# Kernel optimization log

Measured on AMD Instinct MI355X. Metric: run time of the kernel, lower is better.

Reference implementation:

```python
import jax, jax.numpy as jnp
import numpy as np

N = 50000
E = 800000
D_IN, D_HID, D_OUT = 128, 128, 64


def setup_inputs() -> dict:
    key = jax.random.key(0)
    ks = jax.random.split(key, 8)
    x = jax.random.normal(ks[0], (N, D_IN), dtype=jnp.float32)
    edge_index = jax.random.randint(ks[1], (2, E), 0, N, dtype=jnp.int64)
    # Glorot-ish init for GCNConv linear weights + zero bias (PyG default bias=True)
    def lin(k, din, dout):
        s = 1.0 / np.sqrt(din)
        return jax.random.uniform(k, (din, dout), jnp.float32, -s, s)
    return {
        "x": x,
        "edge_index": edge_index,
        "W1": lin(ks[2], D_IN, D_HID), "b1": jnp.zeros((D_HID,), jnp.float32),
        "W2": lin(ks[3], D_HID, D_HID), "b2": jnp.zeros((D_HID,), jnp.float32),
        "W3": lin(ks[4], D_HID, D_OUT), "b3": jnp.zeros((D_OUT,), jnp.float32),
    }


def _prep_edges(edge_index, n):
    # add self loops (PyG GCNConv default add_self_loops=True)
    loop = jnp.arange(n, dtype=edge_index.dtype)
    src = jnp.concatenate([edge_index[0], loop])
    dst = jnp.concatenate([edge_index[1], loop])
    deg = jax.ops.segment_sum(jnp.ones_like(dst, dtype=jnp.float32), dst, num_segments=n)
    dinv = jnp.where(deg > 0, jax.lax.rsqrt(deg), 0.0)
    norm = dinv[src] * dinv[dst]  # symmetric normalization per edge
    return src, dst, norm


def _gcn_conv(h, W, b, src, dst, norm, n):
    h = h @ W                                   # [N, dout]
    msg = h[src] * norm[:, None]                # [E+N, dout] gather
    out = jax.ops.segment_sum(msg, dst, num_segments=n)  # scatter-add
    return out + b


def reference(x, edge_index, W1, b1, W2, b2, W3, b3):
    src, dst, norm = _prep_edges(edge_index, N)
    h = jax.nn.relu(_gcn_conv(x, W1, b1, src, dst, norm, N))
    h = jax.nn.relu(_gcn_conv(h, W2, b2, src, dst, norm, N))
    return _gcn_conv(h, W3, b3, src, dst, norm, N)  # eval mode: dropout is identity
```

## Files before the change

### kernel.cpp

```cpp
#include <hip/hip_runtime.h>
#include <hip/hip_fp16.h>
#include <math.h>

#define NN 50000
#define NE 800000
#define RAWSTRIDE 96
#define NBUCK 196
#define NBBIN 196
#define BCAP 4608
#define ACH 4096
#define G1B 782

using bf8v = __attribute__((ext_vector_type(8))) short;
using f4v  = __attribute__((ext_vector_type(4))) float;
using u32x4 = __attribute__((ext_vector_type(4))) unsigned int;
using u32x2 = __attribute__((ext_vector_type(2))) unsigned int;

__device__ inline unsigned short f2bf(float f) {
    unsigned int u = __float_as_uint(f);
    u += 0x7FFFu + ((u >> 16) & 1u);
    return (unsigned short)(u >> 16);
}
__device__ inline float bflo(unsigned int d) { return __uint_as_float(d << 16); }
__device__ inline float bfhi(unsigned int d) { return __uint_as_float(d & 0xFFFF0000u); }

__device__ inline uint4 ntload4(const void* p) {
    u32x4 v = __builtin_nontemporal_load((const u32x4*)p);
    return make_uint4(v[0], v[1], v[2], v[3]);
}
__device__ inline void ntstore4(void* p, uint4 v) {
    u32x4 x; x[0] = v.x; x[1] = v.y; x[2] = v.z; x[3] = v.w;
    __builtin_nontemporal_store(x, (u32x4*)p);
}
__device__ inline void ntstore2(void* p, uint2 v) {
    u32x2 x; x[0] = v.x; x[1] = v.y;
    __builtin_nontemporal_store(x, (u32x2*)p);
}


__device__ __forceinline__ void bin_body(const int* __restrict__ src,
                                         const int* __restrict__ dst,
                                         int* __restrict__ gcursor,
                                         unsigned int* __restrict__ bst,
                                         int bx, char* shc) {
    unsigned int* items = (unsigned int*)shc;
    int* cnt    = (int*)(shc + 16384);
    int* pref   = (int*)(shc + 17408);
    int* gstart = (int*)(shc + 18436);
    const int t = threadIdx.x;
    cnt[t] = 0;
    __syncthreads();
    const int base = bx * ACH;

    unsigned int my[16]; int myb[16], myr[16];
    #pragma unroll
    for (int i = 0; i < 16; ++i) {
        int e = base + i * 256 + t;
        my[i] = 0; myb[i] = -1; myr[i] = 0;
        if (e < NE) {
            int d = __builtin_nontemporal_load(dst + e);
            int s = __builtin_nontemporal_load(src + e);
            my[i] = (unsigned int)s | ((unsigned int)d << 16);
            int b = d >> 8;
            myb[i] = b;
            myr[i] = atomicAdd(&cnt[b], 1);
        }
    }
    __syncthreads();
    {
        int* scanb = (int*)items;
        scanb[t] = cnt[t];
        __syncthreads();
        #pragma unroll
        for (int off = 1; off < 256; off <<= 1) {
            int v = (t >= off) ? scanb[t - off] : 0;
            __syncthreads();
            scanb[t] += v;
            __syncthreads();
        }
        if (t == 0) pref[0] = 0;
        pref[t + 1] = scanb[t];
    }
    __syncthreads();
    if (cnt[t] > 0) gstart[t] = atomicAdd(&gcursor[t], cnt[t]);
    __syncthreads();
    #pragma unroll
    for (int i = 0; i < 16; ++i)
        if (myb[i] >= 0) items[pref[myb[i]] + myr[i]] = my[i];
    __syncthreads();
    const int total = pref[256];
    for (int i = t; i < total; i += 256) {
        int lo = 0, hi = 255;
        while (lo < hi) { int mid = (lo + hi + 1) >> 1; if (pref[mid] <= i) lo = mid; else hi = mid - 1; }
        int idx = gstart[lo] + (i - pref[lo]);
        if (idx < BCAP) __builtin_nontemporal_store(items[i], &bst[(size_t)lo * BCAP + idx]);
    }
}


__global__ __launch_bounds__(512) void sortb_kernel(const int* __restrict__ gcursor,
                                                    const unsigned int* __restrict__ bst,
                                                    int* __restrict__ cnt_g,
                                                    float* __restrict__ dinv,
                                                    unsigned short* __restrict__ raw) {
    __shared__ unsigned int items[BCAP];
    __shared__ int cnt[256], pref[257], cur[256], scanb[256];
    __shared__ unsigned short outl[BCAP];
    const int b = blockIdx.x;
    const int t = threadIdx.x;
    int n = gcursor[b];
    if (n > BCAP) n = BCAP;
    if (t < 256) { cnt[t] = 0; cur[t] = 0; }
    __syncthreads();
    for (int i = t; i < n; i += 512) {
        unsigned int u = __builtin_nontemporal_load(&bst[(size_t)b * BCAP + i]);
        items[i] = u;
        atomicAdd(&cnt[(u >> 16) & 255], 1);
    }
    __syncthreads();
    if (t < 256) scanb[t] = cnt[t];
    __syncthreads();
    #pragma unroll
    for (int off = 1; off < 256; off <<= 1) {
        int v = 0;
        if (t < 256 && t >= off) v = scanb[t - off];
        __syncthreads();
        if (t < 256) scanb[t] += v;
        __syncthreads();
    }
    if (t == 0) pref[0] = 0;
    if (t < 256) pref[t + 1] = scanb[t];
    __syncthreads();
    for (int i = t; i < n; i += 512) {
        unsigned int u = items[i];
        int ln = (u >> 16) & 255;
        int r = atomicAdd(&cur[ln], 1);
        outl[pref[ln] + r] = (unsigned short)(u & 0xFFFFu);
    }
    __syncthreads();
    for (int i = t; i < n; i += 512) {
        int lo = 0, hi = 255;
        while (lo < hi) { int mid = (lo + hi + 1) >> 1; if (pref[mid] <= i) lo = mid; else hi = mid - 1; }
        int r = i - pref[lo];
        if (r < RAWSTRIDE)
            __builtin_nontemporal_store(outl[i], &raw[(size_t)(b * 256 + lo) * RAWSTRIDE + r]);
    }
    if (t < 256) {
        int node = b * 256 + t;
        if (node < NN) {
            int c = cnt[t];
            cnt_g[node] = c;
            dinv[node] = rsqrtf((float)(1 + c));
        }
    }
}


__device__ __forceinline__ void gemm128_body_f32(const float* __restrict__ A,
                                                 const float* __restrict__ W,
                                                 unsigned short* __restrict__ out,
                                                 int bx, char* shc) {
    unsigned short* Wt = (unsigned short*)shc;
    unsigned short* Dt = (unsigned short*)(shc + 128 * 136 * 2);
    const int t = threadIdx.x;
    const int row0 = bx * 64;

    {
        int n = t & 127;
        int kbase = (t >> 7) * 4;
        for (int kk = kbase; kk < 128; kk += 8) {
            float w0 = W[(kk + 0) * 128 + n];
            float w1 = W[(kk + 1) * 128 + n];
            float w2 = W[(kk + 2) * 128 + n];
            float w3 = W[(kk + 3) * 128 + n];
            unsigned int p0 = (unsigned int)f2bf(w0) | ((unsigned int)f2bf(w1) << 16);
            unsigned int p1 = (unsigned int)f2bf(w2) | ((unsigned int)f2bf(w3) << 16);
            *(unsigned int*)&Wt[n * 136 + kk]     = p0;
            *(unsigned int*)&Wt[n * 136 + kk + 2] = p1;
        }
    }
    __syncthreads();

    const int wave = t >> 6;
    const int lane = t & 63;
    const int m16  = lane & 15;
    const int quad = lane >> 4;
    const int arow = row0 + wave * 16 + m16;
    const int arowc = (arow < NN) ? arow : 0;

    f4v acc[8];
    #pragma unroll
    for (int i = 0; i < 8; ++i) acc[i] = (f4v)(0.0f);

    #pragma unroll
    for (int k0 = 0; k0 < 128; k0 += 32) {
        bf8v afrag;
        const float4* ap = (const float4*)(A + (size_t)arowc * 128 + k0 + quad * 8);
        float4 a0 = ap[0], a1 = ap[1];
        afrag[0] = (short)f2bf(a0.x); afrag[1] = (short)f2bf(a0.y);
        afrag[2] = (short)f2bf(a0.z); afrag[3] = (short)f2bf(a0.w);
        afrag[4] = (short)f2bf(a1.x); afrag[5] = (short)f2bf(a1.y);
        afrag[6] = (short)f2bf(a1.z); afrag[7] = (short)f2bf(a1.w);
        #pragma unroll
        for (int nt = 0; nt < 8; ++nt) {
            bf8v bfrag = *(const bf8v*)&Wt[(nt * 16 + m16) * 136 + k0 + quad * 8];
            acc[nt] = __builtin_amdgcn_mfma_f32_16x16x32_bf16(afrag, bfrag, acc[nt], 0, 0, 0);
        }
    }

    #pragma unroll
    for (int nt = 0; nt < 8; ++nt) {
        #pragma unroll
        for (int r = 0; r < 4; ++r) {
            Dt[(wave * 16 + quad * 4 + r) * 136 + nt * 16 + m16] = f2bf(acc[nt][r]);
        }
    }
    __syncthreads();

    {
        int r = t >> 2;
        int c = t & 3;
        int gr = row0 + r;
        if (gr < NN) {
            const uint4* s = (const uint4*)&Dt[r * 136] + c * 4;
            uint4* d = (uint4*)(out + (size_t)gr * 128) + c * 4;
            ntstore4(d + 0, s[0]); ntstore4(d + 1, s[1]);
            ntstore4(d + 2, s[2]); ntstore4(d + 3, s[3]);
        }
    }
}

__global__ __launch_bounds__(256) void bin_g1_kernel(const int* __restrict__ src,
                                                     const int* __restrict__ dst,
                                                     int* __restrict__ gcursor,
                                                     unsigned int* __restrict__ bst,
                                                     const float* __restrict__ x,
                                                     const float* __restrict__ W1,
                                                     unsigned short* __restrict__ hb) {
    __shared__ __align__(16) char sh[52224];
    if (blockIdx.x < NBBIN) {
        bin_body(src, dst, gcursor, bst, blockIdx.x, sh);
    } else {
        gemm128_body_f32(x, W1, hb, blockIdx.x - NBBIN, sh);
    }
}


#define ACC8(G, W_) \
    acc[0] += W_ * bflo(G.x); acc[1] += W_ * bfhi(G.x); \
    acc[2] += W_ * bflo(G.y); acc[3] += W_ * bfhi(G.y); \
    acc[4] += W_ * bflo(G.z); acc[5] += W_ * bfhi(G.z); \
    acc[6] += W_ * bflo(G.w); acc[7] += W_ * bfhi(G.w);

#define AGG128_BODY(HV, RROW, C, DIW, LANE)                                         \
    {                                                                               \
        uint4 g = HV[(size_t)wid * 16 + (LANE)];                                    \
        float ws = (DIW) * (DIW);                                                   \
        acc[0] = ws * bflo(g.x); acc[1] = ws * bfhi(g.x);                           \
        acc[2] = ws * bflo(g.y); acc[3] = ws * bfhi(g.y);                           \
        acc[4] = ws * bflo(g.z); acc[5] = ws * bfhi(g.z);                           \
        acc[6] = ws * bflo(g.w); acc[7] = ws * bfhi(g.w);                           \
    }                                                                               \
    const int cfull = (C) & ~7;                                                     \
    uint4 q;                                                                        \
    if (cfull > 0) q = ntload4(RROW);                                               \
    for (int e = 0; e < cfull; e += 8) {                                            \
        uint4 qc = q;                                                               \
        if (e + 8 < cfull) q = ntload4((RROW) + e + 8);                             \
        int c0 = qc.x & 0xFFFFu, c1 = qc.x >> 16;                                   \
        int c2 = qc.y & 0xFFFFu, c3 = qc.y >> 16;                                   \
        int c4 = qc.z & 0xFFFFu, c5 = qc.z >> 16;                                   \
        int c6 = qc.w & 0xFFFFu, c7 = qc.w >> 16;                                   \
        uint4 g0 = HV[(size_t)c0 * 16 + (LANE)];                                    \
        uint4 g1 = HV[(size_t)c1 * 16 + (LANE)];                                    \
        uint4 g2 = HV[(size_t)c2 * 16 + (LANE)];                                    \
        uint4 g3 = HV[(size_t)c3 * 16 + (LANE)];                                    \
        uint4 g4 = HV[(size_t)c4 * 16 + (LANE)];                                    \
        uint4 g5 = HV[(size_t)c5 * 16 + (LANE)];                                    \
        uint4 g6 = HV[(size_t)c6 * 16 + (LANE)];                                    \
        uint4 g7 = HV[(size_t)c7 * 16 + (LANE)];                                    \
        float w0 = (DIW) * dinv[c0], w1 = (DIW) * dinv[c1];                         \
        float w2 = (DIW) * dinv[c2], w3 = (DIW) * dinv[c3];                         \
        float w4 = (DIW) * dinv[c4], w5 = (DIW) * dinv[c5];                         \
        float w6 = (DIW) * dinv[c6], w7 = (DIW) * dinv[c7];                         \
        ACC8(g0, w0) ACC8(g1, w1) ACC8(g2, w2) ACC8(g3, w3)                         \
        ACC8(g4, w4) ACC8(g5, w5) ACC8(g6, w6) ACC8(g7, w7)                         \
    }                                                                               \
    if ((C) & 7) {                                                                  \
        int e = cfull, rem = (C) - e;                                               \
        uint4 qc = ntload4((RROW) + e);                                             \
        int c0 = qc.x & 0xFFFFu, c1 = qc.x >> 16;                                   \
        int c2 = qc.y & 0xFFFFu, c3 = qc.y >> 16;                                   \
        int c4 = qc.z & 0xFFFFu, c5 = qc.z >> 16;                                   \
        int c6 = qc.w & 0xFFFFu, c7 = qc.w >> 16;                                   \
        if (rem <= 1) c1 = 0; if (rem <= 2) c2 = 0; if (rem <= 3) c3 = 0;           \
        if (rem <= 4) c4 = 0; if (rem <= 5) c5 = 0; if (rem <= 6) c6 = 0;           \
        c7 = 0;                                                                     \
        float w0 = (DIW) * dinv[c0];                                                \
        float w1 = (rem > 1) ? (DIW) * dinv[c1] : 0.f;                              \
        float w2 = (rem > 2) ? (DIW) * dinv[c2] : 0.f;                              \
        float w3 = (rem > 3) ? (DIW) * dinv[c3] : 0.f;                              \
        float w4 = (rem > 4) ? (DIW) * dinv[c4] : 0.f;                              \
        float w5 = (rem > 5) ? (DIW) * dinv[c5] : 0.f;                              \
        float w6 = (rem > 6) ? (DIW) * dinv[c6] : 0.f;                              \
        float w7 = 0.f;                                                             \
        uint4 g0 = HV[(size_t)c0 * 16 + (LANE)];                                    \
        uint4 g1 = HV[(size_t)c1 * 16 + (LANE)];                                    \
        uint4 g2 = HV[(size_t)c2 * 16 + (LANE)];                                    \
        uint4 g3 = HV[(size_t)c3 * 16 + (LANE)];                                    \
        uint4 g4 = HV[(size_t)c4 * 16 + (LANE)];                                    \
        uint4 g5 = HV[(size_t)c5 * 16 + (LANE)];                                    \
        uint4 g6 = HV[(size_t)c6 * 16 + (LANE)];                                    \
        uint4 g7 = HV[(size_t)c7 * 16 + (LANE)];                                    \
        ACC8(g0, w0) ACC8(g1, w1) ACC8(g2, w2) ACC8(g3, w3)                         \
        ACC8(g4, w4) ACC8(g5, w5) ACC8(g6, w6) ACC8(g7, w7)                         \
    }


__global__ __launch_bounds__(256) void aggW2_kernel(const unsigned short* __restrict__ hin,
                                                    const unsigned short* __restrict__ raw,
                                                    const int* __restrict__ cnt_g,
                                                    const float* __restrict__ dinv,
                                                    const float* __restrict__ bias,
                                                    const float* __restrict__ W,
                                                    unsigned short* __restrict__ out) {
    __shared__ unsigned short Wt[128 * 136];
    __shared__ unsigned short Zt[64 * 136];
    const int t = threadIdx.x;
    const int row0 = blockIdx.x * 64;

    {
        int n = t & 127;
        int kbase = (t >> 7) * 4;
        for (int kk = kbase; kk < 128; kk += 8) {
            float w0 = W[(kk + 0) * 128 + n];
            float w1 = W[(kk + 1) * 128 + n];
            float w2 = W[(kk + 2) * 128 + n];
            float w3 = W[(kk + 3) * 128 + n];
            unsigned int p0 = (unsigned int)f2bf(w0) | ((unsigned int)f2bf(w1) << 16);
            unsigned int p1 = (unsigned int)f2bf(w2) | ((unsigned int)f2bf(w3) << 16);
            *(unsigned int*)&Wt[n * 136 + kk]     = p0;
            *(unsigned int*)&Wt[n * 136 + kk + 2] = p1;
        }
    }

    const int group = t >> 4;
    const int lane  = t & 15;
    const uint4* hv = (const uint4*)hin;
    const float4* bp = (const float4*)bias;
    float4 b0 = bp[lane * 2], b1 = bp[lane * 2 + 1];

    for (int r = 0; r < 4; ++r) {
        const int wid = row0 + r * 16 + group;
        uint4 o = make_uint4(0u, 0u, 0u, 0u);
        if (wid < NN) {
            int c = cnt_g[wid];
            if (c > RAWSTRIDE) c = RAWSTRIDE;
            const float diw = dinv[wid];
            const unsigned short* rrow = raw + (size_t)wid * RAWSTRIDE;
            float acc[8];
            AGG128_BODY(hv, rrow, c, diw, lane)
            acc[0] += b0.x; acc[1] += b0.y; acc[2] += b0.z; acc[3] += b0.w;
            acc[4] += b1.x; acc[5] += b1.y; acc[6] += b1.z; acc[7] += b1.w;
            #pragma unroll
            for (int j = 0; j < 8; ++j) acc[j] = fmaxf(acc[j], 0.f);
            o.x = (unsigned int)f2bf(acc[0]) | ((unsigned int)f2bf(acc[1]) << 16);
            o.y = (unsigned int)f2bf(acc[2]) | ((unsigned int)f2bf(acc[3]) << 16);
            o.z = (unsigned int)f2bf(acc[4]) | ((unsigned int)f2bf(acc[5]) << 16);
            o.w = (unsigned int)f2bf(acc[6]) | ((unsigned int)f2bf(acc[7]) << 16);
        }
        *(uint4*)&Zt[(r * 16 + group) * 136 + lane * 8] = o;
    }
    __syncthreads();

    const int wave = t >> 6;
    const int l64  = t & 63;
    const int m16  = l64 & 15;
    const int quad = l64 >> 4;

    f4v acc[8];
    #pragma unroll
    for (int i = 0; i < 8; ++i) acc[i] = (f4v)(0.0f);

    #pragma unroll
    for (int k0 = 0; k0 < 128; k0 += 32) {
        bf8v afrag = *(const bf8v*)&Zt[(wave * 16 + m16) * 136 + k0 + quad * 8];
        #pragma unroll
        for (int nt = 0; nt < 8; ++nt) {
            bf8v bfrag = *(const bf8v*)&Wt[(nt * 16 + m16) * 136 + k0 + quad * 8];
            acc[nt] = __builtin_amdgcn_mfma_f32_16x16x32_bf16(afrag, bfrag, acc[nt], 0, 0, 0);
        }
    }
    __syncthreads();

    #pragma unroll
    for (int nt = 0; nt < 8; ++nt) {
        #pragma unroll
        for (int r = 0; r < 4; ++r) {
            Zt[(wave * 16 + quad * 4 + r) * 136 + nt * 16 + m16] = f2bf(acc[nt][r]);
        }
    }
    __syncthreads();

    {
        int r = t >> 2;
        int c = t & 3;
        int gr = row0 + r;
        if (gr < NN) {
            const uint4* s = (const uint4*)&Zt[r * 136] + c * 4;
            uint4* d = (uint4*)(out + (size_t)gr * 128) + c * 4;
            ntstore4(d + 0, s[0]); ntstore4(d + 1, s[1]);
            ntstore4(d + 2, s[2]); ntstore4(d + 3, s[3]);
        }
    }
}


__global__ __launch_bounds__(256) void aggG3_kernel(const unsigned short* __restrict__ hin,
                                                    const unsigned short* __restrict__ raw,
                                                    const int* __restrict__ cnt_g,
                                                    const float* __restrict__ dinv,
                                                    const float* __restrict__ bias,
                                                    const float* __restrict__ W,
                                                    unsigned short* __restrict__ outh) {
    constexpr int LD = 132;
    __shared__ float Zt[64 * LD];
    const int t = threadIdx.x;
    const int row0 = blockIdx.x * 64;

    const int group = t >> 4;
    const int lane  = t & 15;
    const uint4* hv = (const uint4*)hin;
    const float4* bp = (const float4*)bias;
    float4 b0 = bp[lane * 2], b1 = bp[lane * 2 + 1];

    for (int r = 0; r < 4; ++r) {
        const int wid = row0 + r * 16 + group;
        float accw[8] = {0.f, 0.f, 0.f, 0.f, 0.f, 0.f, 0.f, 0.f};
        if (wid < NN) {
            int c = cnt_g[wid];
            if (c > RAWSTRIDE) c = RAWSTRIDE;
            const float diw = dinv[wid];
            const unsigned short* rrow = raw + (size_t)wid * RAWSTRIDE;
            float acc[8];
            AGG128_BODY(hv, rrow, c, diw, lane)
            acc[0] += b0.x; acc[1] += b0.y; acc[2] += b0.z; acc[3] += b0.w;
            acc[4] += b1.x; acc[5] += b1.y; acc[6] += b1.z; acc[7] += b1.w;
            #pragma unroll
            for (int j = 0; j < 8; ++j) accw[j] = fmaxf(acc[j], 0.f);
        }
        float4* zr = (float4*)&Zt[(r * 16 + group) * LD + lane * 8];
        zr[0] = make_float4(accw[0], accw[1], accw[2], accw[3]);
        zr[1] = make_float4(accw[4], accw[5], accw[6], accw[7]);
    }
    __syncthreads();

    constexpr int CG = 16;
    constexpr int RPT = 4;
    const int cg = t % CG;
    const int rt = t / CG;
    const float4* Wv = (const float4*)W;
    float4 acc[RPT];
    #pragma unroll
    for (int i = 0; i < RPT; ++i) acc[i] = make_float4(0.f, 0.f, 0.f, 0.f);

    for (int k0 = 0; k0 < 128; k0 += 4) {
        float4 w0 = Wv[(k0 + 0) * CG + cg];
        float4 w1 = Wv[(k0 + 1) * CG + cg];
        float4 w2 = Wv[(k0 + 2) * CG + cg];
        float4 w3 = Wv[(k0 + 3) * CG + cg];
        #pragma unroll
        for (int i = 0; i < RPT; ++i) {
            const float* lr = Zt + (rt * RPT + i) * LD;
            float4 a = ((const float4*)lr)[k0 >> 2];
            acc[i].x += a.x * w0.x + a.y * w1.x + a.z * w2.x + a.w * w3.x;
            acc[i].y += a.x * w0.y + a.y * w1.y + a.z * w2.y + a.w * w3.y;
            acc[i].z += a.x * w0.z + a.y * w1.z + a.z * w2.z + a.w * w3.z;
            acc[i].w += a.x * w0.w + a.y * w1.w + a.z * w2.w + a.w * w3.w;
        }
    }

    #pragma unroll
    for (int i = 0; i < RPT; ++i) {
        int gr = row0 + rt * RPT + i;
        if (gr < NN) {
            uint2 o;
            o.x = (unsigned int)f2bf(acc[i].x) | ((unsigned int)f2bf(acc[i].y) << 16);
            o.y = (unsigned int)f2bf(acc[i].z) | ((unsigned int)f2bf(acc[i].w) << 16);
            ntstore2((uint2*)(outh + (size_t)gr * 64) + cg, o);
        }
    }
}


__global__ __launch_bounds__(256) void agg3_kernel(const unsigned short* __restrict__ hin,
                                                   const unsigned short* __restrict__ raw,
                                                   const int* __restrict__ cnt_g,
                                                   const float* __restrict__ dinv,
                                                   const float* __restrict__ bias,
                                                   float* __restrict__ out) {
    const int t = threadIdx.x;
    const int group = t >> 3;
    const int lane  = t & 7;
    const int wid = blockIdx.x * 32 + group;
    if (wid >= NN) return;

    int c = cnt_g[wid];
    if (c > RAWSTRIDE) c = RAWSTRIDE;
    const float diw = dinv[wid];
    const unsigned short* rrow = raw + (size_t)wid * RAWSTRIDE;
    const uint4* hv = (const uint4*)hin;

    float acc[8];
    {
        uint4 g = hv[(size_t)wid * 8 + lane];
        float ws = diw * diw;
        acc[0] = ws * bflo(g.x); acc[1] = ws * bfhi(g.x);
        acc[2] = ws * bflo(g.y); acc[3] = ws * bfhi(g.y);
        acc[4] = ws * bflo(g.z); acc[5] = ws * bfhi(g.z);
        acc[6] = ws * bflo(g.w); acc[7] = ws * bfhi(g.w);
    }

    const int cfull = c & ~7;
    uint4 q;
    if (cfull > 0) q = ntload4(rrow);
    for (int e = 0; e < cfull; e += 8) {
        uint4 qc = q;
        if (e + 8 < cfull) q = ntload4(rrow + e + 8);
        int c0 = qc.x & 0xFFFFu, c1 = qc.x >> 16;
        int c2 = qc.y & 0xFFFFu, c3 = qc.y >> 16;
        int c4 = qc.z & 0xFFFFu, c5 = qc.z >> 16;
        int c6 = qc.w & 0xFFFFu, c7 = qc.w >> 16;
        uint4 g0 = hv[(size_t)c0 * 8 + lane];
        uint4 g1 = hv[(size_t)c1 * 8 + lane];
        uint4 g2 = hv[(size_t)c2 * 8 + lane];
        uint4 g3 = hv[(size_t)c3 * 8 + lane];
        uint4 g4 = hv[(size_t)c4 * 8 + lane];
        uint4 g5 = hv[(size_t)c5 * 8 + lane];
        uint4 g6 = hv[(size_t)c6 * 8 + lane];
        uint4 g7 = hv[(size_t)c7 * 8 + lane];
        float w0 = diw * dinv[c0], w1 = diw * dinv[c1];
        float w2 = diw * dinv[c2], w3 = diw * dinv[c3];
        float w4 = diw * dinv[c4], w5 = diw * dinv[c5];
        float w6 = diw * dinv[c6], w7 = diw * dinv[c7];
        ACC8(g0, w0) ACC8(g1, w1) ACC8(g2, w2) ACC8(g3, w3)
        ACC8(g4, w4) ACC8(g5, w5) ACC8(g6, w6) ACC8(g7, w7)
    }
    if (c & 7) {
        int e = cfull, rem = c - e;
        uint4 qc = ntload4(rrow + e);
        int c0 = qc.x & 0xFFFFu, c1 = qc.x >> 16;
        int c2 = qc.y & 0xFFFFu, c3 = qc.y >> 16;
        int c4 = qc.z & 0xFFFFu, c5 = qc.z >> 16;
        int c6 = qc.w & 0xFFFFu, c7 = qc.w >> 16;
        if (rem <= 1) c1 = 0; if (rem <= 2) c2 = 0; if (rem <= 3) c3 = 0;
        if (rem <= 4) c4 = 0; if (rem <= 5) c5 = 0; if (rem <= 6) c6 = 0;
        c7 = 0;
        float w0 = diw * dinv[c0];
        float w1 = (rem > 1) ? diw * dinv[c1] : 0.f;
        float w2 = (rem > 2) ? diw * dinv[c2] : 0.f;
        float w3 = (rem > 3) ? diw * dinv[c3] : 0.f;
        float w4 = (rem > 4) ? diw * dinv[c4] : 0.f;
        float w5 = (rem > 5) ? diw * dinv[c5] : 0.f;
        float w6 = (rem > 6) ? diw * dinv[c6] : 0.f;
        float w7 = 0.f;
        uint4 g0 = hv[(size_t)c0 * 8 + lane];
        uint4 g1 = hv[(size_t)c1 * 8 + lane];
        uint4 g2 = hv[(size_t)c2 * 8 + lane];
        uint4 g3 = hv[(size_t)c3 * 8 + lane];
        uint4 g4 = hv[(size_t)c4 * 8 + lane];
        uint4 g5 = hv[(size_t)c5 * 8 + lane];
        uint4 g6 = hv[(size_t)c6 * 8 + lane];
        uint4 g7 = hv[(size_t)c7 * 8 + lane];
        ACC8(g0, w0) ACC8(g1, w1) ACC8(g2, w2) ACC8(g3, w3)
        ACC8(g4, w4) ACC8(g5, w5) ACC8(g6, w6) ACC8(g7, w7)
    }

    const float4* bp = (const float4*)bias;
    float4 b0 = bp[lane * 2], b1 = bp[lane * 2 + 1];
    acc[0] += b0.x; acc[1] += b0.y; acc[2] += b0.z; acc[3] += b0.w;
    acc[4] += b1.x; acc[5] += b1.y; acc[6] += b1.z; acc[7] += b1.w;

    float4 o0 = make_float4(acc[0], acc[1], acc[2], acc[3]);
    float4 o1 = make_float4(acc[4], acc[5], acc[6], acc[7]);
    ((float4*)(out + (size_t)wid * 64))[lane * 2]     = o0;
    ((float4*)(out + (size_t)wid * 64))[lane * 2 + 1] = o1;
}


extern "C" void kernel_launch(void* const* d_in, const int* in_sizes, int n_in,
                              void* d_out, int out_size, void* d_ws, size_t ws_size,
                              hipStream_t stream) {
    const float* x  = (const float*)d_in[0];
    const int*   ei = (const int*)d_in[1];
    const float* W1 = (const float*)d_in[2];
    const float* b1 = (const float*)d_in[3];
    const float* W2 = (const float*)d_in[4];
    const float* b2 = (const float*)d_in[5];
    const float* W3 = (const float*)d_in[6];
    const float* b3 = (const float*)d_in[7];
    float* out = (float*)d_out;

    char* w = (char*)d_ws;
    int*   cnt_g   = (int*)  (w + 0x0000000);
    int*   gcursor = (int*)  (w + 0x0040000);
    float* dinv    = (float*)(w + 0x0048000);
    unsigned int*   bst = (unsigned int*)  (w + 0x0080000);
    unsigned short* raw = (unsigned short*)(w + 0x0400000);
    unsigned short* hb  = (unsigned short*)(w + 0x0E00000);
    unsigned short* h2b = (unsigned short*)(w + 0x1B00000);
    unsigned short* h3b = (unsigned short*)(w + 0x2800000);

    const int* src = ei;
    const int* dst = ei + NE;

    hipMemsetAsync(gcursor, 0, NBUCK * sizeof(int), stream);
    bin_g1_kernel<<<NBBIN + G1B, 256, 0, stream>>>(src, dst, gcursor, bst, x, W1, hb);
    sortb_kernel<<<NBUCK, 512, 0, stream>>>(gcursor, bst, cnt_g, dinv, raw);
    aggW2_kernel<<<G1B, 256, 0, stream>>>(hb, raw, cnt_g, dinv, b1, W2, h2b);
    aggG3_kernel<<<G1B, 256, 0, stream>>>(h2b, raw, cnt_g, dinv, b2, W3, h3b);
    agg3_kernel<<<(NN + 31) / 32, 256, 0, stream>>>(h3b, raw, cnt_g, dinv, b3, out);
}
```

Before: 263.4 us.

## Drop nontemporal loads/stores and write adjacency rows with per-node vector stores

```diff
diff --git a/kernel.cpp b/kernel.cpp
--- a/kernel.cpp
+++ b/kernel.cpp
@@ -13,8 +13,6 @@
 
 using bf8v = __attribute__((ext_vector_type(8))) short;
 using f4v  = __attribute__((ext_vector_type(4))) float;
-using u32x4 = __attribute__((ext_vector_type(4))) unsigned int;
-using u32x2 = __attribute__((ext_vector_type(2))) unsigned int;
 
 __device__ inline unsigned short f2bf(float f) {
     unsigned int u = __float_as_uint(f);
@@ -23,19 +21,6 @@
 }
 __device__ inline float bflo(unsigned int d) { return __uint_as_float(d << 16); }
 __device__ inline float bfhi(unsigned int d) { return __uint_as_float(d & 0xFFFF0000u); }
-
-__device__ inline uint4 ntload4(const void* p) {
-    u32x4 v = __builtin_nontemporal_load((const u32x4*)p);
-    return make_uint4(v[0], v[1], v[2], v[3]);
-}
-__device__ inline void ntstore4(void* p, uint4 v) {
-    u32x4 x; x[0] = v.x; x[1] = v.y; x[2] = v.z; x[3] = v.w;
-    __builtin_nontemporal_store(x, (u32x4*)p);
-}
-__device__ inline void ntstore2(void* p, uint2 v) {
-    u32x2 x; x[0] = v.x; x[1] = v.y;
-    __builtin_nontemporal_store(x, (u32x2*)p);
-}
 
 
 __device__ __forceinline__ void bin_body(const int* __restrict__ src,
@@ -58,8 +43,7 @@
         int e = base + i * 256 + t;
         my[i] = 0; myb[i] = -1; myr[i] = 0;
         if (e < NE) {
-            int d = __builtin_nontemporal_load(dst + e);
-            int s = __builtin_nontemporal_load(src + e);
+            int d = dst[e], s = src[e];
             my[i] = (unsigned int)s | ((unsigned int)d << 16);
             int b = d >> 8;
             myb[i] = b;
@@ -93,7 +77,7 @@
         int lo = 0, hi = 255;
         while (lo < hi) { int mid = (lo + hi + 1) >> 1; if (pref[mid] <= i) lo = mid; else hi = mid - 1; }
         int idx = gstart[lo] + (i - pref[lo]);
-        if (idx < BCAP) __builtin_nontemporal_store(items[i], &bst[(size_t)lo * BCAP + idx]);
+        if (idx < BCAP) bst[(size_t)lo * BCAP + idx] = items[i];
     }
 }
 
@@ -113,7 +97,7 @@
     if (t < 256) { cnt[t] = 0; cur[t] = 0; }
     __syncthreads();
     for (int i = t; i < n; i += 512) {
-        unsigned int u = __builtin_nontemporal_load(&bst[(size_t)b * BCAP + i]);
+        unsigned int u = bst[(size_t)b * BCAP + i];
         items[i] = u;
         atomicAdd(&cnt[(u >> 16) & 255], 1);
     }
@@ -138,14 +122,21 @@
         outl[pref[ln] + r] = (unsigned short)(u & 0xFFFFu);
     }
     __syncthreads();
-    for (int i = t; i < n; i += 512) {
-        int lo = 0, hi = 255;
-        while (lo < hi) { int mid = (lo + hi + 1) >> 1; if (pref[mid] <= i) lo = mid; else hi = mid - 1; }
-        int r = i - pref[lo];
-        if (r < RAWSTRIDE)
-            __builtin_nontemporal_store(outl[i], &raw[(size_t)(b * 256 + lo) * RAWSTRIDE + r]);
-    }
     if (t < 256) {
+        int start = pref[t];
+        int cn = pref[t + 1] - start;
+        if (cn > RAWSTRIDE) cn = RAWSTRIDE;
+        unsigned short* drow = raw + (size_t)(b * 256 + t) * RAWSTRIDE;
+        int i = 0;
+        for (; i + 8 <= cn; i += 8) {
+            uint4 v;
+            v.x = (unsigned int)outl[start + i]     | ((unsigned int)outl[start + i + 1] << 16);
+            v.y = (unsigned int)outl[start + i + 2] | ((unsigned int)outl[start + i + 3] << 16);
+            v.z = (unsigned int)outl[start + i + 4] | ((unsigned int)outl[start + i + 5] << 16);
+            v.w = (unsigned int)outl[start + i + 6] | ((unsigned int)outl[start + i + 7] << 16);
+            *(uint4*)(drow + i) = v;
+        }
+        for (; i < cn; ++i) drow[i] = outl[start + i];
         int node = b * 256 + t;
         if (node < NN) {
             int c = cnt[t];
@@ -224,8 +215,7 @@
         if (gr < NN) {
             const uint4* s = (const uint4*)&Dt[r * 136] + c * 4;
             uint4* d = (uint4*)(out + (size_t)gr * 128) + c * 4;
-            ntstore4(d + 0, s[0]); ntstore4(d + 1, s[1]);
-            ntstore4(d + 2, s[2]); ntstore4(d + 3, s[3]);
+            d[0] = s[0]; d[1] = s[1]; d[2] = s[2]; d[3] = s[3];
         }
     }
 }
@@ -263,10 +253,10 @@
     }                                                                               \
     const int cfull = (C) & ~7;                                                     \
     uint4 q;                                                                        \
-    if (cfull > 0) q = ntload4(RROW);                                               \
+    if (cfull > 0) q = *(const uint4*)(RROW);                                       \
     for (int e = 0; e < cfull; e += 8) {                                            \
         uint4 qc = q;                                                               \
-        if (e + 8 < cfull) q = ntload4((RROW) + e + 8);                             \
+        if (e + 8 < cfull) q = *(const uint4*)((RROW) + e + 8);                     \
         int c0 = qc.x & 0xFFFFu, c1 = qc.x >> 16;                                   \
         int c2 = qc.y & 0xFFFFu, c3 = qc.y >> 16;                                   \
         int c4 = qc.z & 0xFFFFu, c5 = qc.z >> 16;                                   \
@@ -288,7 +278,7 @@
     }                                                                               \
     if ((C) & 7) {                                                                  \
         int e = cfull, rem = (C) - e;                                               \
-        uint4 qc = ntload4((RROW) + e);                                             \
+        uint4 qc = *(const uint4*)((RROW) + e);                                     \
         int c0 = qc.x & 0xFFFFu, c1 = qc.x >> 16;                                   \
         int c2 = qc.y & 0xFFFFu, c3 = qc.y >> 16;                                   \
         int c4 = qc.z & 0xFFFFu, c5 = qc.z >> 16;                                   \
@@ -409,8 +399,7 @@
         if (gr < NN) {
             const uint4* s = (const uint4*)&Zt[r * 136] + c * 4;
             uint4* d = (uint4*)(out + (size_t)gr * 128) + c * 4;
-            ntstore4(d + 0, s[0]); ntstore4(d + 1, s[1]);
-            ntstore4(d + 2, s[2]); ntstore4(d + 3, s[3]);
+            d[0] = s[0]; d[1] = s[1]; d[2] = s[2]; d[3] = s[3];
         }
     }
 }
@@ -487,7 +476,7 @@
             uint2 o;
             o.x = (unsigned int)f2bf(acc[i].x) | ((unsigned int)f2bf(acc[i].y) << 16);
             o.y = (unsigned int)f2bf(acc[i].z) | ((unsigned int)f2bf(acc[i].w) << 16);
-            ntstore2((uint2*)(outh + (size_t)gr * 64) + cg, o);
+            ((uint2*)(outh + (size_t)gr * 64))[cg] = o;
         }
     }
 }
@@ -523,10 +512,10 @@
 
     const int cfull = c & ~7;
     uint4 q;
-    if (cfull > 0) q = ntload4(rrow);
+    if (cfull > 0) q = *(const uint4*)(rrow);
     for (int e = 0; e < cfull; e += 8) {
         uint4 qc = q;
-        if (e + 8 < cfull) q = ntload4(rrow + e + 8);
+        if (e + 8 < cfull) q = *(const uint4*)(rrow + e + 8);
         int c0 = qc.x & 0xFFFFu, c1 = qc.x >> 16;
         int c2 = qc.y & 0xFFFFu, c3 = qc.y >> 16;
         int c4 = qc.z & 0xFFFFu, c5 = qc.z >> 16;
@@ -548,7 +537,7 @@
     }
     if (c & 7) {
         int e = cfull, rem = c - e;
-        uint4 qc = ntload4(rrow + e);
+        uint4 qc = *(const uint4*)(rrow + e);
         int c0 = qc.x & 0xFFFFu, c1 = qc.x >> 16;
         int c2 = qc.y & 0xFFFFu, c3 = qc.y >> 16;
         int c4 = qc.z & 0xFFFFu, c5 = qc.z >> 16;
```

Measured after the change: 232.6 us. -11.7%, faster.
